# Performance work log

Hardware: AMD Instinct MI355X
Metric: run time of the kernel (lower is better)

The kernel has to match this reference:

```python
import jax, jax.numpy as jnp
import numpy as np

B, H, S, D = 4, 16, 2048, 64

def setup_inputs() -> dict:
    key = jax.random.key(0)
    kq, kk, kv = jax.random.split(key, 3)
    q = jax.random.normal(kq, (B, H, S, D), dtype=jnp.float32)
    k = jax.random.normal(kk, (B, H, S, D), dtype=jnp.float32)
    v = jax.random.normal(kv, (B, H, S, D), dtype=jnp.float32)
    scale = jnp.float32(np.sqrt(D))  # 8.0
    return {"q": q, "k": k, "v": v, "scale": scale}

def reference(q, k, v, scale):
    # scores: [B,H,S,S] = (Q @ K^T) / scale
    scores = jnp.einsum('bhqd,bhkd->bhqk', q, k) / scale
    probs = jax.nn.softmax(scores, axis=-1)
    # dropout p=0.0 in eval-equivalent reference -> identity
    out = jnp.einsum('bhqk,bhkd->bhqd', probs, v)
    return out
```

## Files before the change

### kernel.cpp

```cpp
#include <hip/hip_runtime.h>

#define Sq 2048
#define Dq 64
#define NH 64
#define KVBLK 64
#define NKVIT (Sq / KVBLK)
#define PT_STRIDE 72

#define QBLK_P 128
#define NQB_P (Sq / QBLK_P)
#define NBLK_P (NH * NQB_P)

#define QBLK 64
#define NQB (Sq / QBLK)
#define NBLK (NH * NQB)

#define TILE_ELEMS 4096
#define IMG_TILES (NH * NKVIT)
#define IMG_BYTES ((size_t)IMG_TILES * TILE_ELEMS * 2)
#define WS_IMG_OFF 4096
#define WS_NEEDED (WS_IMG_OFF + 2 * IMG_BYTES)

#define QK_SCALE (0.125f * 1.44269504088896f)
#define DEFER_THR 8.0f

typedef __attribute__((ext_vector_type(8))) short bf16x8;
typedef __attribute__((ext_vector_type(4))) float f32x4;

__device__ __forceinline__ float bflo(unsigned int u) {
    union { unsigned int i; float f; } x; x.i = u << 16; return x.f;
}
__device__ __forceinline__ unsigned int f2bf(float f) {
    union { float f; unsigned int i; } x; x.f = f;
    return (x.i + 0x7fffu + ((x.i >> 16) & 1u)) >> 16;
}
__device__ __forceinline__ unsigned int cvtpk(float lo, float hi) {
    unsigned int r;
    asm("v_cvt_pk_bf16_f32 %0, %1, %2" : "=v"(r) : "v"(lo), "v"(hi));
    return r;
}

__global__ void detect_dtype(const unsigned int* __restrict__ Q,
                             int* __restrict__ flag) {
    unsigned int u = Q[threadIdx.x];
    float a = fabsf(bflo(u));
    bool sane = (a >= 9.3e-10f) && (a <= 64.0f);
    unsigned long long b = __ballot(sane);
    if (threadIdx.x == 0) *flag = (__builtin_popcountll(b) >= 48) ? 1 : 0;
}

__device__ __forceinline__ void gload_lds16(const unsigned short* g, unsigned short* l) {
    __builtin_amdgcn_global_load_lds(
        (const __attribute__((address_space(1))) void*)g,
        (__attribute__((address_space(3))) void*)l, 16, 0, 0);
}

__device__ __forceinline__ int vt_swz(int d, int kv) {
    return (d * KVBLK + kv) ^ ((((d & 7) ^ ((d >> 3) & 7))) << 3);
}

__global__ __launch_bounds__(256) void convert_kv(
    const float* __restrict__ K, const float* __restrict__ V,
    unsigned short* __restrict__ img, const int* __restrict__ flag)
{
    if (*flag) return;
    __shared__ __align__(16) unsigned short VtL[TILE_ELEMS];

    const int tile = (int)blockIdx.x;
    const int tid  = threadIdx.x;
    const size_t gbase = (size_t)tile * (KVBLK * Dq);

    unsigned short* kim = img + (size_t)tile * TILE_ELEMS;
    unsigned short* vtg = img + (size_t)(IMG_TILES + tile) * TILE_ELEMS;

    const float4* kt4 = (const float4*)(K + gbase);
    const float4* vt4 = (const float4*)(V + gbase);

    #pragma unroll
    for (int c = 0; c < 4; ++c) {
        const int r  = (c * 256 + tid) >> 4;
        const int c0 = (tid & 15) * 4;
        {
            float4 u4 = kt4[c * 256 + tid];
            unsigned int p0 = f2bf(u4.x) | (f2bf(u4.y) << 16);
            unsigned int p1 = f2bf(u4.z) | (f2bf(u4.w) << 16);
            const int sw = c0 ^ ((r & 7) << 3);
            *(uint2*)(kim + r * 64 + sw) = make_uint2(p0, p1);
        }
        {
            float4 u4 = vt4[c * 256 + tid];
            float xs[4] = {u4.x, u4.y, u4.z, u4.w};
            #pragma unroll
            for (int e = 0; e < 4; ++e)
                VtL[vt_swz(c0 + e, r)] = (unsigned short)f2bf(xs[e]);
        }
    }
    __syncthreads();
    #pragma unroll
    for (int c = 0; c < 2; ++c)
        *(uint4*)(vtg + (c * 256 + tid) * 8) = *(const uint4*)(VtL + (c * 256 + tid) * 8);
}

#define SOFTMAX_BODY(SACC, MR, OA, LA)                                          \
{                                                                               \
    float rmax[4];                                                              \
    _Pragma("unroll")                                                           \
    for (int r = 0; r < 4; ++r)                                                 \
        rmax[r] = fmaxf(fmaxf(SACC[0][r], SACC[1][r]),                          \
                        fmaxf(SACC[2][r], SACC[3][r]));                         \
    bool grow = (rmax[0] > MR[0] + DEFER_THR) | (rmax[1] > MR[1] + DEFER_THR)   \
              | (rmax[2] > MR[2] + DEFER_THR) | (rmax[3] > MR[3] + DEFER_THR);  \
    if (__any(grow)) {                                                          \
        f32x4 av;                                                               \
        _Pragma("unroll")                                                       \
        for (int r = 0; r < 4; ++r) {                                           \
            float t = rmax[r];                                                  \
            _Pragma("unroll")                                                   \
            for (int msk = 1; msk <= 8; msk <<= 1)                              \
                t = fmaxf(t, __shfl_xor(t, msk, 64));                           \
            float mnew = fmaxf(MR[r], t);                                       \
            av[r] = exp2f(MR[r] - mnew);                                        \
            MR[r] = mnew;                                                       \
        }                                                                       \
        _Pragma("unroll")                                                       \
        for (int dt = 0; dt < 4; ++dt) OA[dt] *= av;                            \
        LA *= av;                                                               \
    }                                                                           \
    _Pragma("unroll")                                                           \
    for (int nt = 0; nt < 4; ++nt) {                                            \
        _Pragma("unroll")                                                       \
        for (int r = 0; r < 4; ++r)                                             \
            SACC[nt][r] = exp2f(SACC[nt][r] - MR[r]);                           \
    }                                                                           \
}

__global__ __launch_bounds__(256, 3) void fa_mfma_f32_pre(
    const float* __restrict__ Q, const unsigned short* __restrict__ img,
    float* __restrict__ O, const int* __restrict__ flag)
{
    if (*flag) return;

    __shared__ __align__(16) unsigned short Kt[2][TILE_ELEMS];
    __shared__ __align__(16) unsigned short Vt[2][TILE_ELEMS];
    __shared__ __align__(16) unsigned short Pl[4][16 * PT_STRIDE];

    const int tid  = threadIdx.x;
    const int lane = tid & 63;
    const int w    = tid >> 6;
    const int l15  = lane & 15;
    const int lg   = lane >> 4;

    const int bid  = (int)blockIdx.x;
    const int blk  = (bid & 7) * (NBLK_P / 8) + (bid >> 3);
    const int head = blk >> 4;
    const int q0   = (blk & 15) * QBLK_P;
    const size_t hb = (size_t)head * (Sq * Dq);

    bf16x8 qh[2][2], ql[2][2];
    #pragma unroll
    for (int m = 0; m < 2; ++m) {
        const float4* qv = (const float4*)(Q + hb
            + (size_t)(q0 + w * 32 + m * 16 + l15) * Dq + lg * 8);
        #pragma unroll
        for (int s = 0; s < 2; ++s) {
            float xs[8];
            #pragma unroll
            for (int j4 = 0; j4 < 2; ++j4) {
                float4 u = qv[s * 8 + j4];
                xs[j4*4+0]=u.x; xs[j4*4+1]=u.y; xs[j4*4+2]=u.z; xs[j4*4+3]=u.w;
            }
            #pragma unroll
            for (int j = 0; j < 8; ++j) {
                float x = xs[j] * QK_SCALE;
                unsigned int u = __float_as_uint(x);
                float hf = __uint_as_float(u & 0xffff0000u);
                qh[m][s][j] = (short)(u >> 16);
                ql[m][s][j] = (short)(__float_as_uint(x - hf) >> 16);
            }
        }
    }

    bf16x8 onesb;
    #pragma unroll
    for (int j = 0; j < 8; ++j) onesb[j] = (short)0x3F80;

    f32x4 oacc0[4], oacc1[4];
    #pragma unroll
    for (int dt = 0; dt < 4; ++dt) {
        oacc0[dt] = (f32x4){0.f, 0.f, 0.f, 0.f};
        oacc1[dt] = (f32x4){0.f, 0.f, 0.f, 0.f};
    }
    f32x4 lacc0 = (f32x4){0.f,0.f,0.f,0.f}, lacc1 = (f32x4){0.f,0.f,0.f,0.f};
    float mrow0[4], mrow1[4];
    #pragma unroll
    for (int r = 0; r < 4; ++r) { mrow0[r] = -1e30f; mrow1[r] = -1e30f; }

    const unsigned short* kim_h = img + (size_t)(head * NKVIT) * TILE_ELEMS;
    const unsigned short* vtg_h = img + (size_t)(IMG_TILES + head * NKVIT) * TILE_ELEMS;

    #define STAGE(T, B)                                                 \
    {                                                                   \
        const size_t toff_ = (size_t)(T) * TILE_ELEMS;                  \
        _Pragma("unroll")                                               \
        for (int c_ = 0; c_ < 2; ++c_) {                                \
            const int e8_ = (c_ * 256 + tid) * 8;                       \
            gload_lds16(kim_h + toff_ + e8_, &Kt[B][e8_]);              \
            gload_lds16(vtg_h + toff_ + e8_, &Vt[B][e8_]);              \
        }                                                               \
    }

    STAGE(0, 0)

    for (int it = 0; it < NKVIT; ++it) {
        const int cur = it & 1;
        asm volatile("s_waitcnt vmcnt(0)" ::: "memory");
        __syncthreads();
        if (it + 1 < NKVIT) STAGE(it + 1, cur ^ 1)

        const unsigned short* KtC = &Kt[cur][0];
        const unsigned short* VtC = &Vt[cur][0];

        f32x4 s0[4], s1[4];
        #pragma unroll
        for (int nt = 0; nt < 4; ++nt) {
            s0[nt] = (f32x4){0.f,0.f,0.f,0.f};
            s1[nt] = (f32x4){0.f,0.f,0.f,0.f};
        }
        __builtin_amdgcn_s_setprio(1);
        #pragma unroll
        for (int s = 0; s < 2; ++s) {
            #pragma unroll
            for (int nt = 0; nt < 4; ++nt) {
                const int n = nt * 16 + l15;
                const int off = n * 64 + ((s * 32 + lg * 8) ^ ((n & 7) << 3));
                bf16x8 kf = *(const bf16x8*)(KtC + off);
                s0[nt] = __builtin_amdgcn_mfma_f32_16x16x32_bf16(qh[0][s], kf, s0[nt], 0, 0, 0);
                s0[nt] = __builtin_amdgcn_mfma_f32_16x16x32_bf16(ql[0][s], kf, s0[nt], 0, 0, 0);
                s1[nt] = __builtin_amdgcn_mfma_f32_16x16x32_bf16(qh[1][s], kf, s1[nt], 0, 0, 0);
                s1[nt] = __builtin_amdgcn_mfma_f32_16x16x32_bf16(ql[1][s], kf, s1[nt], 0, 0, 0);
            }
        }
        __builtin_amdgcn_s_setprio(0);

        SOFTMAX_BODY(s0, mrow0, oacc0, lacc0)
        SOFTMAX_BODY(s1, mrow1, oacc1, lacc1)

        unsigned short* pw = &Pl[w][0];
        bf16x8 pf0[2], pf1[2];
        #pragma unroll
        for (int nt = 0; nt < 4; ++nt) {
            const int cc = nt * 16 + l15;
            unsigned int ua = cvtpk(s0[nt][0], s0[nt][1]);
            unsigned int ub = cvtpk(s0[nt][2], s0[nt][3]);
            pw[(lg * 4 + 0) * PT_STRIDE + cc] = (unsigned short)(ua & 0xffffu);
            pw[(lg * 4 + 1) * PT_STRIDE + cc] = (unsigned short)(ua >> 16);
            pw[(lg * 4 + 2) * PT_STRIDE + cc] = (unsigned short)(ub & 0xffffu);
            pw[(lg * 4 + 3) * PT_STRIDE + cc] = (unsigned short)(ub >> 16);
        }
        #pragma unroll
        for (int s2 = 0; s2 < 2; ++s2)
            pf0[s2] = *(const bf16x8*)(pw + l15 * PT_STRIDE + s2 * 32 + lg * 8);
        #pragma unroll
        for (int nt = 0; nt < 4; ++nt) {
            const int cc = nt * 16 + l15;
            unsigned int ua = cvtpk(s1[nt][0], s1[nt][1]);
            unsigned int ub = cvtpk(s1[nt][2], s1[nt][3]);
            pw[(lg * 4 + 0) * PT_STRIDE + cc] = (unsigned short)(ua & 0xffffu);
            pw[(lg * 4 + 1) * PT_STRIDE + cc] = (unsigned short)(ua >> 16);
            pw[(lg * 4 + 2) * PT_STRIDE + cc] = (unsigned short)(ub & 0xffffu);
            pw[(lg * 4 + 3) * PT_STRIDE + cc] = (unsigned short)(ub >> 16);
        }
        #pragma unroll
        for (int s2 = 0; s2 < 2; ++s2)
            pf1[s2] = *(const bf16x8*)(pw + l15 * PT_STRIDE + s2 * 32 + lg * 8);

        __builtin_amdgcn_s_setprio(1);
        #pragma unroll
        for (int s2 = 0; s2 < 2; ++s2) {
            lacc0 = __builtin_amdgcn_mfma_f32_16x16x32_bf16(pf0[s2], onesb, lacc0, 0, 0, 0);
            lacc1 = __builtin_amdgcn_mfma_f32_16x16x32_bf16(pf1[s2], onesb, lacc1, 0, 0, 0);
            #pragma unroll
            for (int dt = 0; dt < 4; ++dt) {
                const int d = dt * 16 + l15;
                bf16x8 vf = *(const bf16x8*)(VtC + vt_swz(d, s2 * 32 + lg * 8));
                oacc0[dt] = __builtin_amdgcn_mfma_f32_16x16x32_bf16(pf0[s2], vf, oacc0[dt], 0, 0, 0);
                oacc1[dt] = __builtin_amdgcn_mfma_f32_16x16x32_bf16(pf1[s2], vf, oacc1[dt], 0, 0, 0);
            }
        }
        __builtin_amdgcn_s_setprio(0);
    }
    #undef STAGE

    {
        float inv[4];
        #pragma unroll
        for (int r = 0; r < 4; ++r) inv[r] = 1.f / lacc0[r];
        float* ob = O + hb + (size_t)(q0 + w * 32) * Dq;
        #pragma unroll
        for (int dt = 0; dt < 4; ++dt) {
            #pragma unroll
            for (int r = 0; r < 4; ++r)
                ob[(size_t)(lg * 4 + r) * Dq + dt * 16 + l15] = oacc0[dt][r] * inv[r];
        }
    }
    {
        float inv[4];
        #pragma unroll
        for (int r = 0; r < 4; ++r) inv[r] = 1.f / lacc1[r];
        float* ob = O + hb + (size_t)(q0 + w * 32 + 16) * Dq;
        #pragma unroll
        for (int dt = 0; dt < 4; ++dt) {
            #pragma unroll
            for (int r = 0; r < 4; ++r)
                ob[(size_t)(lg * 4 + r) * Dq + dt * 16 + l15] = oacc1[dt][r] * inv[r];
        }
    }
}

__global__ __launch_bounds__(256, 2) void fa_mfma_f32_fused(
    const float* __restrict__ Q, const float* __restrict__ K,
    const float* __restrict__ V, float* __restrict__ O,
    const int* __restrict__ flag)
{
    if (*flag) return;

    __shared__ __align__(16) unsigned short Kh[KVBLK * Dq];
    __shared__ __align__(16) unsigned short Kl[KVBLK * Dq];
    __shared__ __align__(16) unsigned short Vt[Dq * KVBLK];
    __shared__ __align__(16) unsigned short Pl[4][16 * PT_STRIDE];

    const int tid  = threadIdx.x;
    const int lane = tid & 63;
    const int w    = tid >> 6;
    const int l15  = lane & 15;
    const int lg   = lane >> 4;

    const int bid  = (int)blockIdx.x;
    const int blk  = (bid & 7) * (NBLK / 8) + (bid >> 3);
    const int head = blk >> 5;
    const int q0   = (blk & 31) * QBLK;
    const size_t hb = (size_t)head * (Sq * Dq);

    bf16x8 qh[2], ql[2];
    {
        const float* qp = Q + hb + (size_t)(q0 + w * 16 + l15) * Dq + lg * 8;
        #pragma unroll
        for (int s = 0; s < 2; ++s) {
            #pragma unroll
            for (int j = 0; j < 8; ++j) {
                float x = qp[s * 32 + j] * 0.125f;
                unsigned int u = __float_as_uint(x);
                float hf = __uint_as_float(u & 0xffff0000u);
                qh[s][j] = (short)(u >> 16);
                ql[s][j] = (short)(__float_as_uint(x - hf) >> 16);
            }
        }
    }

    f32x4 oacc[4];
    #pragma unroll
    for (int dt = 0; dt < 4; ++dt) oacc[dt] = (f32x4){0.f, 0.f, 0.f, 0.f};
    float mrow[4], lrow[4];
    #pragma unroll
    for (int r = 0; r < 4; ++r) { mrow[r] = -1e30f; lrow[r] = 0.f; }

    const float* kbase = K + hb;
    const float* vbase = V + hb;

    float4 kr[4], vr[4];
    {
        const float4* kt4 = (const float4*)kbase;
        const float4* vt4 = (const float4*)vbase;
        #pragma unroll
        for (int c = 0; c < 4; ++c) { kr[c] = kt4[c * 256 + tid]; vr[c] = vt4[c * 256 + tid]; }
    }

    for (int it = 0; it < NKVIT; ++it) {
        __syncthreads();
        #pragma unroll
        for (int c = 0; c < 4; ++c) {
            const int r  = c * 16 + (tid >> 4);
            const int c0 = (tid & 15) * 4;
            const int sw = c0 ^ ((r & 7) << 3);
            float xs[4] = {kr[c].x, kr[c].y, kr[c].z, kr[c].w};
            unsigned int hp[2], lp[2];
            #pragma unroll
            for (int e = 0; e < 2; ++e) {
                unsigned int u0 = __float_as_uint(xs[2*e]);
                unsigned int u1 = __float_as_uint(xs[2*e+1]);
                hp[e] = (u0 >> 16) | (u1 & 0xffff0000u);
                float h0 = __uint_as_float(u0 & 0xffff0000u);
                float h1 = __uint_as_float(u1 & 0xffff0000u);
                lp[e] = (__float_as_uint(xs[2*e] - h0) >> 16)
                      | (__float_as_uint(xs[2*e+1] - h1) & 0xffff0000u);
            }
            *(uint2*)(Kh + r * 64 + sw) = make_uint2(hp[0], hp[1]);
            *(uint2*)(Kl + r * 64 + sw) = make_uint2(lp[0], lp[1]);
        }
        #pragma unroll
        for (int c = 0; c < 4; ++c) {
            const int kv = c * 16 + (tid >> 4);
            const int d0 = (tid & 15) * 4;
            float xs[4] = {vr[c].x, vr[c].y, vr[c].z, vr[c].w};
            #pragma unroll
            for (int e = 0; e < 4; ++e)
                Vt[vt_swz(d0 + e, kv)] = (unsigned short)f2bf(xs[e]);
        }
        __syncthreads();

        if (it + 1 < NKVIT) {
            const float4* kt4 = (const float4*)(kbase + (size_t)(it + 1) * KVBLK * Dq);
            const float4* vt4 = (const float4*)(vbase + (size_t)(it + 1) * KVBLK * Dq);
            #pragma unroll
            for (int c = 0; c < 4; ++c) { kr[c] = kt4[c * 256 + tid]; vr[c] = vt4[c * 256 + tid]; }
        }

        f32x4 sacc[4];
        #pragma unroll
        for (int nt = 0; nt < 4; ++nt) sacc[nt] = (f32x4){0.f, 0.f, 0.f, 0.f};
        #pragma unroll
        for (int s = 0; s < 2; ++s) {
            #pragma unroll
            for (int nt = 0; nt < 4; ++nt) {
                const int n = nt * 16 + l15;
                const int off = n * 64 + ((s * 32 + lg * 8) ^ ((n & 7) << 3));
                bf16x8 khf = *(const bf16x8*)(Kh + off);
                bf16x8 klf = *(const bf16x8*)(Kl + off);
                sacc[nt] = __builtin_amdgcn_mfma_f32_16x16x32_bf16(qh[s], khf, sacc[nt], 0, 0, 0);
                sacc[nt] = __builtin_amdgcn_mfma_f32_16x16x32_bf16(qh[s], klf, sacc[nt], 0, 0, 0);
                sacc[nt] = __builtin_amdgcn_mfma_f32_16x16x32_bf16(ql[s], khf, sacc[nt], 0, 0, 0);
            }
        }

        float mnew[4], alpha[4];
        #pragma unroll
        for (int r = 0; r < 4; ++r) {
            float t = fmaxf(fmaxf(sacc[0][r], sacc[1][r]), fmaxf(sacc[2][r], sacc[3][r]));
            #pragma unroll
            for (int msk = 1; msk <= 8; msk <<= 1)
                t = fmaxf(t, __shfl_xor(t, msk, 64));
            mnew[r]  = fmaxf(mrow[r], t);
            alpha[r] = __expf(mrow[r] - mnew[r]);
            mrow[r]  = mnew[r];
        }
        float psum[4] = {0.f, 0.f, 0.f, 0.f};
        #pragma unroll
        for (int nt = 0; nt < 4; ++nt) {
            #pragma unroll
            for (int r = 0; r < 4; ++r) {
                float p = __expf(sacc[nt][r] - mnew[r]);
                sacc[nt][r] = p;
                psum[r] += p;
            }
        }
        #pragma unroll
        for (int r = 0; r < 4; ++r) {
            float t = psum[r];
            #pragma unroll
            for (int msk = 1; msk <= 8; msk <<= 1)
                t += __shfl_xor(t, msk, 64);
            lrow[r] = lrow[r] * alpha[r] + t;
        }
        {
            f32x4 av; av[0] = alpha[0]; av[1] = alpha[1]; av[2] = alpha[2]; av[3] = alpha[3];
            #pragma unroll
            for (int dt = 0; dt < 4; ++dt) oacc[dt] *= av;
        }

        unsigned short* pw = &Pl[w][0];
        #pragma unroll
        for (int nt = 0; nt < 4; ++nt) {
            const int cc = nt * 16 + l15;
            #pragma unroll
            for (int r = 0; r < 4; ++r)
                pw[(lg * 4 + r) * PT_STRIDE + cc] = (unsigned short)f2bf(sacc[nt][r]);
        }

        #pragma unroll
        for (int s2 = 0; s2 < 2; ++s2) {
            bf16x8 pf = *(const bf16x8*)(pw + l15 * PT_STRIDE + s2 * 32 + lg * 8);
            #pragma unroll
            for (int dt = 0; dt < 4; ++dt) {
                const int d = dt * 16 + l15;
                bf16x8 vf = *(const bf16x8*)(Vt + vt_swz(d, s2 * 32 + lg * 8));
                oacc[dt] = __builtin_amdgcn_mfma_f32_16x16x32_bf16(pf, vf, oacc[dt], 0, 0, 0);
            }
        }
    }

    float inv4[4];
    #pragma unroll
    for (int r = 0; r < 4; ++r) inv4[r] = 1.f / lrow[r];
    float* ob = O + hb + (size_t)(q0 + w * 16) * Dq;
    #pragma unroll
    for (int dt = 0; dt < 4; ++dt) {
        #pragma unroll
        for (int r = 0; r < 4; ++r)
            ob[(size_t)(lg * 4 + r) * Dq + dt * 16 + l15] = oacc[dt][r] * inv4[r];
    }
}

__global__ __launch_bounds__(256, 3) void fa_mfma_bf16(
    const unsigned short* __restrict__ Q, const unsigned short* __restrict__ K,
    const unsigned short* __restrict__ V, unsigned short* __restrict__ O,
    const int* __restrict__ flag)
{
    if (!(*flag)) return;

    __shared__ __align__(16) unsigned short Kt[KVBLK * Dq];
    __shared__ __align__(16) unsigned short Vt[Dq * KVBLK];
    __shared__ __align__(16) unsigned short Pl[4][16 * PT_STRIDE];

    const int tid  = threadIdx.x;
    const int lane = tid & 63;
    const int w    = tid >> 6;
    const int l15  = lane & 15;
    const int lg   = lane >> 4;

    const int bid  = (int)blockIdx.x;
    const int blk  = (bid & 7) * (NBLK / 8) + (bid >> 3);
    const int head = blk >> 5;
    const int q0   = (blk & 31) * QBLK;
    const size_t hb = (size_t)head * (Sq * Dq);

    bf16x8 qf[2];
    {
        const bf16x8* qp = (const bf16x8*)(Q + hb + (size_t)(q0 + w * 16 + l15) * Dq);
        qf[0] = qp[lg];
        qf[1] = qp[4 + lg];
    }

    f32x4 oacc[4];
    #pragma unroll
    for (int dt = 0; dt < 4; ++dt) oacc[dt] = (f32x4){0.f, 0.f, 0.f, 0.f};
    float mrow[4], lrow[4];
    #pragma unroll
    for (int r = 0; r < 4; ++r) { mrow[r] = -1e30f; lrow[r] = 0.f; }

    const int sr = tid >> 3;
    const int sc = tid & 7;
    const int kswz_elem = (sc * 8) ^ ((sr & 7) << 3);

    for (int it = 0; it < NKVIT; ++it) {
        const int kv0 = it * KVBLK;
        __syncthreads();
        #pragma unroll
        for (int c = 0; c < 2; ++c) {
            gload_lds16(K + hb + (size_t)(kv0 + c * 32 + sr) * Dq + kswz_elem,
                        Kt + c * 2048 + tid * 8);
        }
        uint4 vreg[2];
        #pragma unroll
        for (int c = 0; c < 2; ++c)
            vreg[c] = *(const uint4*)(V + hb + (size_t)(kv0 + c * 32 + sr) * Dq + sc * 8);

        asm volatile("s_waitcnt vmcnt(0)" ::: "memory");

        #pragma unroll
        for (int c = 0; c < 2; ++c) {
            const int kv = c * 32 + sr;
            unsigned int vu[4] = { vreg[c].x, vreg[c].y, vreg[c].z, vreg[c].w };
            #pragma unroll
            for (int e2 = 0; e2 < 4; ++e2) {
                const int d0 = sc * 8 + e2 * 2;
                Vt[vt_swz(d0,     kv)] = (unsigned short)(vu[e2] & 0xffffu);
                Vt[vt_swz(d0 + 1, kv)] = (unsigned short)(vu[e2] >> 16);
            }
        }
        __syncthreads();

        f32x4 sacc[4];
        #pragma unroll
        for (int nt = 0; nt < 4; ++nt) sacc[nt] = (f32x4){0.f, 0.f, 0.f, 0.f};
        #pragma unroll
        for (int s = 0; s < 2; ++s) {
            #pragma unroll
            for (int nt = 0; nt < 4; ++nt) {
                const int n = nt * 16 + l15;
                bf16x8 kf = *(const bf16x8*)(Kt + n * 64 + ((s * 32 + lg * 8) ^ ((n & 7) << 3)));
                sacc[nt] = __builtin_amdgcn_mfma_f32_16x16x32_bf16(qf[s], kf, sacc[nt], 0, 0, 0);
            }
        }
        #pragma unroll
        for (int nt = 0; nt < 4; ++nt) sacc[nt] *= 0.125f;

        float mnew[4], alpha[4];
        #pragma unroll
        for (int r = 0; r < 4; ++r) {
            float t = fmaxf(fmaxf(sacc[0][r], sacc[1][r]), fmaxf(sacc[2][r], sacc[3][r]));
            #pragma unroll
            for (int msk = 1; msk <= 8; msk <<= 1)
                t = fmaxf(t, __shfl_xor(t, msk, 64));
            mnew[r]  = fmaxf(mrow[r], t);
            alpha[r] = __expf(mrow[r] - mnew[r]);
            mrow[r]  = mnew[r];
        }
        float psum[4] = {0.f, 0.f, 0.f, 0.f};
        #pragma unroll
        for (int nt = 0; nt < 4; ++nt) {
            #pragma unroll
            for (int r = 0; r < 4; ++r) {
                float p = __expf(sacc[nt][r] - mnew[r]);
                sacc[nt][r] = p;
                psum[r] += p;
            }
        }
        #pragma unroll
        for (int r = 0; r < 4; ++r) {
            float t = psum[r];
            #pragma unroll
            for (int msk = 1; msk <= 8; msk <<= 1)
                t += __shfl_xor(t, msk, 64);
            lrow[r] = lrow[r] * alpha[r] + t;
        }
        {
            f32x4 av; av[0] = alpha[0]; av[1] = alpha[1]; av[2] = alpha[2]; av[3] = alpha[3];
            #pragma unroll
            for (int dt = 0; dt < 4; ++dt) oacc[dt] *= av;
        }

        unsigned short* pw = &Pl[w][0];
        #pragma unroll
        for (int nt = 0; nt < 4; ++nt) {
            const int cc = nt * 16 + l15;
            #pragma unroll
            for (int r = 0; r < 4; ++r)
                pw[(lg * 4 + r) * PT_STRIDE + cc] = (unsigned short)f2bf(sacc[nt][r]);
        }

        #pragma unroll
        for (int s2 = 0; s2 < 2; ++s2) {
            bf16x8 pf = *(const bf16x8*)(pw + l15 * PT_STRIDE + s2 * 32 + lg * 8);
            #pragma unroll
            for (int dt = 0; dt < 4; ++dt) {
                const int d = dt * 16 + l15;
                bf16x8 vf = *(const bf16x8*)(Vt + vt_swz(d, s2 * 32 + lg * 8));
                oacc[dt] = __builtin_amdgcn_mfma_f32_16x16x32_bf16(pf, vf, oacc[dt], 0, 0, 0);
            }
        }
    }

    float inv4[4];
    #pragma unroll
    for (int r = 0; r < 4; ++r) inv4[r] = 1.f / lrow[r];
    unsigned short* ob = O + (size_t)(head * Sq + q0 + w * 16) * Dq;
    #pragma unroll
    for (int dt = 0; dt < 4; ++dt) {
        #pragma unroll
        for (int r = 0; r < 4; ++r)
            ob[(size_t)(lg * 4 + r) * Dq + dt * 16 + l15] = (unsigned short)f2bf(oacc[dt][r] * inv4[r]);
    }
}

extern "C" void kernel_launch(void* const* d_in, const int* in_sizes, int n_in,
                              void* d_out, int out_size, void* d_ws, size_t ws_size,
                              hipStream_t stream) {
    int* flag = (int*)d_ws;
    detect_dtype<<<dim3(1), dim3(64), 0, stream>>>((const unsigned int*)d_in[0], flag);
    if (ws_size >= WS_NEEDED) {
        unsigned short* img = (unsigned short*)((char*)d_ws + WS_IMG_OFF);
        convert_kv<<<dim3(IMG_TILES), dim3(256), 0, stream>>>(
            (const float*)d_in[1], (const float*)d_in[2], img, flag);
        fa_mfma_f32_pre<<<dim3(NBLK_P), dim3(256), 0, stream>>>(
            (const float*)d_in[0], img, (float*)d_out, flag);
    } else {
        fa_mfma_f32_fused<<<dim3(NBLK), dim3(256), 0, stream>>>(
            (const float*)d_in[0], (const float*)d_in[1],
            (const float*)d_in[2], (float*)d_out, flag);
    }
    fa_mfma_bf16<<<dim3(NBLK), dim3(256), 0, stream>>>(
        (const unsigned short*)d_in[0], (const unsigned short*)d_in[1],
        (const unsigned short*)d_in[2], (unsigned short*)d_out, flag);
}
```

Measured before the change: 285.2 us.

## Transpose MFMA operands so P stays in registers, dropping LDS round-trip

Swaps the operand order of the QK^T and PV MFMAs so scores come out transposed: each lane holds one query row's values. K rows are permuted so the accumulator layout of S^T matches the B-operand layout needed for the PV product. This lets the kernel pack P directly into bf16 registers and skip the per-wave LDS staging buffer and its stores and reloads. Row max now needs only two cross-lane shuffles, and the output is written with float4 stores. The risk is that the K-row permutation must match the MFMA register layout exactly, or results will be wrong.

```diff
diff --git a/kernel.cpp b/kernel.cpp
--- a/kernel.cpp
+++ b/kernel.cpp
@@ -101,39 +101,6 @@
         *(uint4*)(vtg + (c * 256 + tid) * 8) = *(const uint4*)(VtL + (c * 256 + tid) * 8);
 }
 
-#define SOFTMAX_BODY(SACC, MR, OA, LA)                                          \
-{                                                                               \
-    float rmax[4];                                                              \
-    _Pragma("unroll")                                                           \
-    for (int r = 0; r < 4; ++r)                                                 \
-        rmax[r] = fmaxf(fmaxf(SACC[0][r], SACC[1][r]),                          \
-                        fmaxf(SACC[2][r], SACC[3][r]));                         \
-    bool grow = (rmax[0] > MR[0] + DEFER_THR) | (rmax[1] > MR[1] + DEFER_THR)   \
-              | (rmax[2] > MR[2] + DEFER_THR) | (rmax[3] > MR[3] + DEFER_THR);  \
-    if (__any(grow)) {                                                          \
-        f32x4 av;                                                               \
-        _Pragma("unroll")                                                       \
-        for (int r = 0; r < 4; ++r) {                                           \
-            float t = rmax[r];                                                  \
-            _Pragma("unroll")                                                   \
-            for (int msk = 1; msk <= 8; msk <<= 1)                              \
-                t = fmaxf(t, __shfl_xor(t, msk, 64));                           \
-            float mnew = fmaxf(MR[r], t);                                       \
-            av[r] = exp2f(MR[r] - mnew);                                        \
-            MR[r] = mnew;                                                       \
-        }                                                                       \
-        _Pragma("unroll")                                                       \
-        for (int dt = 0; dt < 4; ++dt) OA[dt] *= av;                            \
-        LA *= av;                                                               \
-    }                                                                           \
-    _Pragma("unroll")                                                           \
-    for (int nt = 0; nt < 4; ++nt) {                                            \
-        _Pragma("unroll")                                                       \
-        for (int r = 0; r < 4; ++r)                                             \
-            SACC[nt][r] = exp2f(SACC[nt][r] - MR[r]);                           \
-    }                                                                           \
-}
-
 __global__ __launch_bounds__(256, 3) void fa_mfma_f32_pre(
     const float* __restrict__ Q, const unsigned short* __restrict__ img,
     float* __restrict__ O, const int* __restrict__ flag)
@@ -142,7 +109,6 @@
 
     __shared__ __align__(16) unsigned short Kt[2][TILE_ELEMS];
     __shared__ __align__(16) unsigned short Vt[2][TILE_ELEMS];
-    __shared__ __align__(16) unsigned short Pl[4][16 * PT_STRIDE];
 
     const int tid  = threadIdx.x;
     const int lane = tid & 63;
@@ -191,9 +157,7 @@
         oacc1[dt] = (f32x4){0.f, 0.f, 0.f, 0.f};
     }
     f32x4 lacc0 = (f32x4){0.f,0.f,0.f,0.f}, lacc1 = (f32x4){0.f,0.f,0.f,0.f};
-    float mrow0[4], mrow1[4];
-    #pragma unroll
-    for (int r = 0; r < 4; ++r) { mrow0[r] = -1e30f; mrow1[r] = -1e30f; }
+    float m0 = -1e30f, m1 = -1e30f;
 
     const unsigned short* kim_h = img + (size_t)(head * NKVIT) * TILE_ELEMS;
     const unsigned short* vtg_h = img + (size_t)(IMG_TILES + head * NKVIT) * TILE_ELEMS;
@@ -211,6 +175,8 @@
 
     STAGE(0, 0)
 
+    const int krb = ((l15 >> 2) << 3) + (l15 & 3);
+
     for (int it = 0; it < NKVIT; ++it) {
         const int cur = it & 1;
         asm volatile("s_waitcnt vmcnt(0)" ::: "memory");
@@ -231,88 +197,92 @@
         for (int s = 0; s < 2; ++s) {
             #pragma unroll
             for (int nt = 0; nt < 4; ++nt) {
-                const int n = nt * 16 + l15;
-                const int off = n * 64 + ((s * 32 + lg * 8) ^ ((n & 7) << 3));
+                const int krow = ((nt & 1) << 5) + ((nt >> 1) << 2) + krb;
+                const int off  = krow * 64 + ((s * 32 + lg * 8) ^ ((krow & 7) << 3));
                 bf16x8 kf = *(const bf16x8*)(KtC + off);
-                s0[nt] = __builtin_amdgcn_mfma_f32_16x16x32_bf16(qh[0][s], kf, s0[nt], 0, 0, 0);
-                s0[nt] = __builtin_amdgcn_mfma_f32_16x16x32_bf16(ql[0][s], kf, s0[nt], 0, 0, 0);
-                s1[nt] = __builtin_amdgcn_mfma_f32_16x16x32_bf16(qh[1][s], kf, s1[nt], 0, 0, 0);
-                s1[nt] = __builtin_amdgcn_mfma_f32_16x16x32_bf16(ql[1][s], kf, s1[nt], 0, 0, 0);
+                s0[nt] = __builtin_amdgcn_mfma_f32_16x16x32_bf16(kf, qh[0][s], s0[nt], 0, 0, 0);
+                s0[nt] = __builtin_amdgcn_mfma_f32_16x16x32_bf16(kf, ql[0][s], s0[nt], 0, 0, 0);
+                s1[nt] = __builtin_amdgcn_mfma_f32_16x16x32_bf16(kf, qh[1][s], s1[nt], 0, 0, 0);
+                s1[nt] = __builtin_amdgcn_mfma_f32_16x16x32_bf16(kf, ql[1][s], s1[nt], 0, 0, 0);
             }
         }
         __builtin_amdgcn_s_setprio(0);
 
-        SOFTMAX_BODY(s0, mrow0, oacc0, lacc0)
-        SOFTMAX_BODY(s1, mrow1, oacc1, lacc1)
-
-        unsigned short* pw = &Pl[w][0];
-        bf16x8 pf0[2], pf1[2];
+        float lm0 = s0[0][0], lm1 = s1[0][0];
         #pragma unroll
         for (int nt = 0; nt < 4; ++nt) {
-            const int cc = nt * 16 + l15;
-            unsigned int ua = cvtpk(s0[nt][0], s0[nt][1]);
-            unsigned int ub = cvtpk(s0[nt][2], s0[nt][3]);
-            pw[(lg * 4 + 0) * PT_STRIDE + cc] = (unsigned short)(ua & 0xffffu);
-            pw[(lg * 4 + 1) * PT_STRIDE + cc] = (unsigned short)(ua >> 16);
-            pw[(lg * 4 + 2) * PT_STRIDE + cc] = (unsigned short)(ub & 0xffffu);
-            pw[(lg * 4 + 3) * PT_STRIDE + cc] = (unsigned short)(ub >> 16);
-        }
-        #pragma unroll
-        for (int s2 = 0; s2 < 2; ++s2)
-            pf0[s2] = *(const bf16x8*)(pw + l15 * PT_STRIDE + s2 * 32 + lg * 8);
+            #pragma unroll
+            for (int r = 0; r < 4; ++r) {
+                lm0 = fmaxf(lm0, s0[nt][r]);
+                lm1 = fmaxf(lm1, s1[nt][r]);
+            }
+        }
+        if (__any((lm0 > m0 + DEFER_THR) | (lm1 > m1 + DEFER_THR))) {
+            float t0 = lm0, t1 = lm1;
+            t0 = fmaxf(t0, __shfl_xor(t0, 16, 64));
+            t0 = fmaxf(t0, __shfl_xor(t0, 32, 64));
+            t1 = fmaxf(t1, __shfl_xor(t1, 16, 64));
+            t1 = fmaxf(t1, __shfl_xor(t1, 32, 64));
+            float n0 = fmaxf(m0, t0), n1 = fmaxf(m1, t1);
+            float a0 = exp2f(m0 - n0);
+            float a1 = exp2f(m1 - n1);
+            m0 = n0; m1 = n1;
+            #pragma unroll
+            for (int dt = 0; dt < 4; ++dt) { oacc0[dt] *= a0; oacc1[dt] *= a1; }
+            lacc0 *= a0; lacc1 *= a1;
+        }
         #pragma unroll
         for (int nt = 0; nt < 4; ++nt) {
-            const int cc = nt * 16 + l15;
-            unsigned int ua = cvtpk(s1[nt][0], s1[nt][1]);
-            unsigned int ub = cvtpk(s1[nt][2], s1[nt][3]);
-            pw[(lg * 4 + 0) * PT_STRIDE + cc] = (unsigned short)(ua & 0xffffu);
-            pw[(lg * 4 + 1) * PT_STRIDE + cc] = (unsigned short)(ua >> 16);
-            pw[(lg * 4 + 2) * PT_STRIDE + cc] = (unsigned short)(ub & 0xffffu);
-            pw[(lg * 4 + 3) * PT_STRIDE + cc] = (unsigned short)(ub >> 16);
-        }
-        #pragma unroll
-        for (int s2 = 0; s2 < 2; ++s2)
-            pf1[s2] = *(const bf16x8*)(pw + l15 * PT_STRIDE + s2 * 32 + lg * 8);
-
-        __builtin_amdgcn_s_setprio(1);
+            #pragma unroll
+            for (int r = 0; r < 4; ++r) {
+                s0[nt][r] = exp2f(s0[nt][r] - m0);
+                s1[nt][r] = exp2f(s1[nt][r] - m1);
+            }
+        }
+
         #pragma unroll
         for (int s2 = 0; s2 < 2; ++s2) {
-            lacc0 = __builtin_amdgcn_mfma_f32_16x16x32_bf16(pf0[s2], onesb, lacc0, 0, 0, 0);
-            lacc1 = __builtin_amdgcn_mfma_f32_16x16x32_bf16(pf1[s2], onesb, lacc1, 0, 0, 0);
+            union { unsigned int u[4]; bf16x8 v; } p0, p1;
+            p0.u[0] = cvtpk(s0[s2    ][0], s0[s2    ][1]);
+            p0.u[1] = cvtpk(s0[s2    ][2], s0[s2    ][3]);
+            p0.u[2] = cvtpk(s0[s2 + 2][0], s0[s2 + 2][1]);
+            p0.u[3] = cvtpk(s0[s2 + 2][2], s0[s2 + 2][3]);
+            p1.u[0] = cvtpk(s1[s2    ][0], s1[s2    ][1]);
+            p1.u[1] = cvtpk(s1[s2    ][2], s1[s2    ][3]);
+            p1.u[2] = cvtpk(s1[s2 + 2][0], s1[s2 + 2][1]);
+            p1.u[3] = cvtpk(s1[s2 + 2][2], s1[s2 + 2][3]);
+            __builtin_amdgcn_s_setprio(1);
+            lacc0 = __builtin_amdgcn_mfma_f32_16x16x32_bf16(onesb, p0.v, lacc0, 0, 0, 0);
+            lacc1 = __builtin_amdgcn_mfma_f32_16x16x32_bf16(onesb, p1.v, lacc1, 0, 0, 0);
             #pragma unroll
             for (int dt = 0; dt < 4; ++dt) {
-                const int d = dt * 16 + l15;
-                bf16x8 vf = *(const bf16x8*)(VtC + vt_swz(d, s2 * 32 + lg * 8));
-                oacc0[dt] = __builtin_amdgcn_mfma_f32_16x16x32_bf16(pf0[s2], vf, oacc0[dt], 0, 0, 0);
-                oacc1[dt] = __builtin_amdgcn_mfma_f32_16x16x32_bf16(pf1[s2], vf, oacc1[dt], 0, 0, 0);
-            }
-        }
-        __builtin_amdgcn_s_setprio(0);
+                bf16x8 vf = *(const bf16x8*)(VtC + vt_swz(dt * 16 + l15, s2 * 32 + lg * 8));
+                oacc0[dt] = __builtin_amdgcn_mfma_f32_16x16x32_bf16(vf, p0.v, oacc0[dt], 0, 0, 0);
+                oacc1[dt] = __builtin_amdgcn_mfma_f32_16x16x32_bf16(vf, p1.v, oacc1[dt], 0, 0, 0);
+            }
+            __builtin_amdgcn_s_setprio(0);
+        }
     }
     #undef STAGE
 
     {
-        float inv[4];
-        #pragma unroll
-        for (int r = 0; r < 4; ++r) inv[r] = 1.f / lacc0[r];
-        float* ob = O + hb + (size_t)(q0 + w * 32) * Dq;
+        const float inv = 1.f / lacc0[0];
+        float* ob = O + hb + (size_t)(q0 + w * 32 + l15) * Dq;
         #pragma unroll
         for (int dt = 0; dt < 4; ++dt) {
-            #pragma unroll
-            for (int r = 0; r < 4; ++r)
-                ob[(size_t)(lg * 4 + r) * Dq + dt * 16 + l15] = oacc0[dt][r] * inv[r];
+            float4 v; v.x = oacc0[dt][0] * inv; v.y = oacc0[dt][1] * inv;
+                      v.z = oacc0[dt][2] * inv; v.w = oacc0[dt][3] * inv;
+            *(float4*)(ob + dt * 16 + lg * 4) = v;
         }
     }
     {
-        float inv[4];
-        #pragma unroll
-        for (int r = 0; r < 4; ++r) inv[r] = 1.f / lacc1[r];
-        float* ob = O + hb + (size_t)(q0 + w * 32 + 16) * Dq;
+        const float inv = 1.f / lacc1[0];
+        float* ob = O + hb + (size_t)(q0 + w * 32 + 16 + l15) * Dq;
         #pragma unroll
         for (int dt = 0; dt < 4; ++dt) {
-            #pragma unroll
-            for (int r = 0; r < 4; ++r)
-                ob[(size_t)(lg * 4 + r) * Dq + dt * 16 + l15] = oacc1[dt][r] * inv[r];
+            float4 v; v.x = oacc1[dt][0] * inv; v.y = oacc1[dt][1] * inv;
+                      v.z = oacc1[dt][2] * inv; v.w = oacc1[dt][3] * inv;
+            *(float4*)(ob + dt * 16 + lg * 4) = v;
         }
     }
 }
```

Measured after the change: 260.2 us. 1.1x faster.
